# Optimization experiments

Measured on AMD Instinct MI355X. Metric: run time of the kernel, lower is better.

## Reference

```python
import jax, jax.numpy as jnp
import numpy as np
import math

H = 8          # num_heads
HD = 16        # head_dim = attention_dim // (2*num_heads) = 256 // 16
E_SUB = 256
E_GENE = 256
DEPTH = 1
LAMBDA_INIT = 0.8 - 0.6 * math.exp(-0.3 * DEPTH)
EPS_SM = 1e-20
EPS_RMS = 1e-5


def setup_inputs() -> dict:
    key = jax.random.key(0)
    ks = jax.random.split(key, 12)
    B, S, P, G = 4, 512, 64, 32
    d2 = 2 * H * HD  # 256
    inp = {
        'query': jax.random.normal(ks[0], (B, S, E_SUB), jnp.float32),
        'key': jax.random.normal(ks[1], (B, P, G, E_GENE), jnp.float32),
        'query_mask': jnp.ones((B, S), dtype=bool),
        'key_mask': jnp.ones((B, P, G), dtype=bool),
        'Wq': jax.random.normal(ks[2], (E_SUB, d2), jnp.float32) / np.sqrt(E_SUB),
        'Wk': jax.random.normal(ks[3], (E_GENE, d2), jnp.float32) / np.sqrt(E_GENE),
        'Wv': jax.random.normal(ks[4], (E_GENE, d2), jnp.float32) / np.sqrt(E_GENE),
        'Wo': jax.random.normal(ks[5], (d2, E_SUB), jnp.float32) / np.sqrt(d2),
        'lq1': 0.1 * jax.random.normal(ks[6], (HD,), jnp.float32),
        'lk1': 0.1 * jax.random.normal(ks[7], (HD,), jnp.float32),
        'lq2': 0.1 * jax.random.normal(ks[8], (HD,), jnp.float32),
        'lk2': 0.1 * jax.random.normal(ks[9], (HD,), jnp.float32),
        'g': jnp.ones((2 * HD,), jnp.float32),  # RMSNorm weight
    }
    return inp


def _stable_softmax(x):
    x = x.astype(jnp.float32)
    m = jnp.max(x, axis=-1, keepdims=True)
    e = jnp.exp(x - m)
    return e / (jnp.sum(e, axis=-1, keepdims=True) + EPS_SM)


def reference(query, key, query_mask, key_mask, Wq, Wk, Wv, Wo, lq1, lk1, lq2, lk2, g):
    B, S, _ = query.shape
    _, P, G, Ek = key.shape
    Lk = P * G
    scaling = HD ** -0.5
    key_flat = key.reshape(B, Lk, Ek)
    # [B, H, 2, S/Lk, HD]
    Q = (query @ Wq).reshape(B, S, H, 2, HD).transpose(0, 2, 3, 1, 4) * scaling
    K = (key_flat @ Wk).reshape(B, Lk, H, 2, HD).transpose(0, 2, 3, 1, 4)
    V = (key_flat @ Wv).reshape(B, Lk, H, 2, HD).transpose(0, 2, 3, 1, 4)
    # dual-slot scores [B, H, 2, S, Lk]
    scores = jnp.einsum('bhtsd,bhtld->bhtsl', Q, K)
    mask = query_mask[:, None, None, :, None] & key_mask.reshape(B, Lk)[:, None, None, None, :]
    scores = jnp.where(mask, scores, jnp.float32(-1e20))
    scores = _stable_softmax(scores)
    lam1 = jnp.exp(jnp.sum(lq1 * lk1))
    lam2 = jnp.exp(jnp.sum(lq2 * lk2))
    lam_full = lam1 - lam2 + LAMBDA_INIT
    diff_attn = scores[:, :, 0] - lam_full * scores[:, :, 1]  # [B,H,S,Lk]
    V_cat = V.transpose(0, 1, 3, 2, 4).reshape(B, H, Lk, 2 * HD)
    out = jnp.einsum('bhsl,bhld->bhsd', diff_attn, V_cat)
    # RMSNorm over last dim, then scale
    rms = jax.lax.rsqrt(jnp.mean(out * out, axis=-1, keepdims=True) + EPS_RMS)
    out = out * rms * g * (1.0 - LAMBDA_INIT)
    out = out.transpose(0, 2, 1, 3).reshape(B, S, 2 * H * HD) @ Wo
    return out, diff_attn.reshape(B, H, S, P, G)
```

## Files before the change

### kernel.cpp

```cpp
#include <hip/hip_runtime.h>
#include <hip/hip_bf16.h>


typedef float  f32x4  __attribute__((ext_vector_type(4)));
typedef float  f32x16 __attribute__((ext_vector_type(16)));
typedef short  s16x8  __attribute__((ext_vector_type(8)));
typedef unsigned short u16;
typedef unsigned short u16x4 __attribute__((ext_vector_type(4)));
typedef unsigned int   u32;

#define LAMBDA_INIT   0.35550906759096926f
#define ONE_MINUS_LI  0.6444909324090307f
#define QSCALE        0.36067376022224085f

__device__ __forceinline__ u16 f2b(float x) {
  unsigned u = __float_as_uint(x);
  u += 0x7FFFu + ((u >> 16) & 1u);
  return (u16)(u >> 16);
}

__device__ __forceinline__ u32 cvtpk(float lo, float hi) {
  u32 r;
  asm("v_cvt_pk_bf16_f32 %0, %1, %2" : "=v"(r) : "v"(lo), "v"(hi));
  return r;
}

__device__ __forceinline__ float fexp2(float x) {
  return __builtin_amdgcn_exp2f(x);
}

__global__ __launch_bounds__(256) void proj_kernel(
    const float* __restrict__ query, const float* __restrict__ key,
    const float* __restrict__ Wq, const float* __restrict__ Wk,
    const float* __restrict__ Wv,
    u16* __restrict__ Qs, u16* __restrict__ Ks, u16* __restrict__ Vt) {
  const int z = blockIdx.z;
  if (z == 0 && blockIdx.x >= 32) return;
  const float* A = (z == 0) ? query : key;
  const float* W = (z == 0) ? Wq : (z == 1) ? Wk : Wv;
  u16*         Out = (z == 0) ? Qs : (z == 1) ? Ks : Vt;
  const float scale = (z == 0) ? QSCALE : 1.0f;

  __shared__ u16 ldsA[64][40];
  __shared__ u16 ldsB[64][40];
  const int m0 = blockIdx.x * 64, n0 = blockIdx.y * 64;
  const int tid = threadIdx.x;
  const int w = tid >> 6, lane = tid & 63;
  const int wm = (w >> 1) * 32, wn = (w & 1) * 32;
  const int c = lane & 15, q = lane >> 4;
  const int lr = tid >> 2, lc = (tid & 3) * 8;
  const int n2 = tid & 63, ko = tid >> 6;
  f32x4 acc[2][2] = {};
  const float* aptr = A + (size_t)(m0 + lr) * 256 + lc;
  const float* bp   = W + (size_t)(ko * 8) * 256 + n0 + n2;

  f32x4 a0 = *reinterpret_cast<const f32x4*>(aptr);
  f32x4 a1 = *reinterpret_cast<const f32x4*>(aptr + 4);
  float bw[8];
#pragma unroll
  for (int j = 0; j < 8; ++j) bw[j] = bp[(size_t)j * 256];
  for (int k0 = 0; k0 < 256; k0 += 32) {
    u16x4 p0 = {f2b(a0[0]), f2b(a0[1]), f2b(a0[2]), f2b(a0[3])};
    u16x4 p1 = {f2b(a1[0]), f2b(a1[1]), f2b(a1[2]), f2b(a1[3])};
    *reinterpret_cast<u16x4*>(&ldsA[lr][lc]) = p0;
    *reinterpret_cast<u16x4*>(&ldsA[lr][lc + 4]) = p1;
    s16x8 pb;
#pragma unroll
    for (int j = 0; j < 8; ++j) pb[j] = (short)f2b(bw[j]);
    *reinterpret_cast<s16x8*>(&ldsB[n2][ko * 8]) = pb;
    __syncthreads();
    if (k0 + 32 < 256) {
      a0 = *reinterpret_cast<const f32x4*>(aptr + k0 + 32);
      a1 = *reinterpret_cast<const f32x4*>(aptr + k0 + 36);
#pragma unroll
      for (int j = 0; j < 8; ++j) bw[j] = bp[(size_t)(k0 + 32 + j) * 256];
    }
    s16x8 af0 = *reinterpret_cast<const s16x8*>(&ldsA[wm + c][q * 8]);
    s16x8 af1 = *reinterpret_cast<const s16x8*>(&ldsA[wm + 16 + c][q * 8]);
    s16x8 bf0 = *reinterpret_cast<const s16x8*>(&ldsB[wn + c][q * 8]);
    s16x8 bf1 = *reinterpret_cast<const s16x8*>(&ldsB[wn + 16 + c][q * 8]);
    acc[0][0] = __builtin_amdgcn_mfma_f32_16x16x32_bf16(af0, bf0, acc[0][0], 0, 0, 0);
    acc[0][1] = __builtin_amdgcn_mfma_f32_16x16x32_bf16(af0, bf1, acc[0][1], 0, 0, 0);
    acc[1][0] = __builtin_amdgcn_mfma_f32_16x16x32_bf16(af1, bf0, acc[1][0], 0, 0, 0);
    acc[1][1] = __builtin_amdgcn_mfma_f32_16x16x32_bf16(af1, bf1, acc[1][1], 0, 0, 0);
    __syncthreads();
  }
#pragma unroll
  for (int mf = 0; mf < 2; ++mf)
#pragma unroll
    for (int nf = 0; nf < 2; ++nf) {
      int m = m0 + wm + mf * 16 + q * 4;
      int n = n0 + wn + nf * 16 + c;
      int hh = n >> 5, dd = n & 31;
      if (z == 2) {
        int bb = m >> 11, l = m & 2047;
        int t = l >> 4, u = l & 15;
        u16x4 pk = {f2b(acc[mf][nf][0]), f2b(acc[mf][nf][1]),
                    f2b(acc[mf][nf][2]), f2b(acc[mf][nf][3])};
        size_t idx = (((size_t)((bb * 8 + hh) * 128 + t)) * 32 + dd) * 16 + u;
        *reinterpret_cast<u16x4*>(Out + idx) = pk;
      } else {
#pragma unroll
        for (int r = 0; r < 4; ++r) {
          int mm = m + r;
          size_t idx;
          if (z == 0) {
            int bb = mm >> 9, s = mm & 511;
            idx = ((size_t)((bb * 8 + hh) * 512 + s)) * 32 + dd;
          } else {
            int bb = mm >> 11, l = mm & 2047;
            idx = ((size_t)((bb * 8 + hh) * 2048 + l)) * 32 + dd;
          }
          Out[idx] = f2b(acc[mf][nf][r] * scale);
        }
      }
    }
}

__global__ __launch_bounds__(512, 4) void attn_fused_kernel(
    const u16* __restrict__ Qs, const u16* __restrict__ Ks,
    const u16* __restrict__ Vt,
    const float* __restrict__ lq1, const float* __restrict__ lk1,
    const float* __restrict__ lq2, const float* __restrict__ lk2,
    const float* __restrict__ g,
    float* __restrict__ diff_out, u16* __restrict__ normed) {
  __shared__ float psum[8][2][32];
  __shared__ float rden[2][32];
  __shared__ float avred[8][16][64];
  __shared__ float pstg[8][32][33];
  const int i = blockIdx.x;
  const int xcd = i & 7, j = i >> 3;
  const int bh = xcd * 4 + (j >> 4);
  const int st = j & 15;
  const int b = bh >> 3, h = bh & 7;
  const int tid = threadIdx.x, w = tid >> 6, lane = tid & 63;
  const int ln = lane & 31, hi = lane >> 5;
  const int lbase = w * 256;

  float a1 = 0.f, a2 = 0.f;
#pragma unroll
  for (int t = 0; t < 16; ++t) { a1 += lq1[t] * lk1[t]; a2 += lq2[t] * lk2[t]; }
  const float lam = expf(a1) - expf(a2) + LAMBDA_INIT;

  const u16* qptr = Qs + ((size_t)((b * 8 + h) * 512 + st * 32 + ln)) * 32 + hi * 8;
  const s16x8 qf0 = *reinterpret_cast<const s16x8*>(qptr);
  const s16x8 qf1 = *reinterpret_cast<const s16x8*>(qptr + 16);
  const u16* kbase = Ks + ((size_t)((b * 8 + h) * 2048)) * 32 + hi * 8;
  const u16* vbase = Vt + ((size_t)(b * 8 + h)) * 65536 + ln * 16 + hi * 8;

  float s0 = 0.f, s1 = 0.f;
  {
    const u16* kptr = kbase + (size_t)(lbase + ln) * 32;
    s16x8 kf0 = *reinterpret_cast<const s16x8*>(kptr);
    s16x8 kf1 = *reinterpret_cast<const s16x8*>(kptr + 16);
    for (int l0 = lbase; l0 < lbase + 256; l0 += 32) {
      const int lnext = (l0 + 32 < lbase + 256) ? l0 + 32 : lbase;
      const u16* knext = kbase + (size_t)(lnext + ln) * 32;
      s16x8 nf0 = *reinterpret_cast<const s16x8*>(knext);
      s16x8 nf1 = *reinterpret_cast<const s16x8*>(knext + 16);
      f32x16 c0 = {}, c1 = {};
      c0 = __builtin_amdgcn_mfma_f32_32x32x16_bf16(kf0, qf0, c0, 0, 0, 0);
      c1 = __builtin_amdgcn_mfma_f32_32x32x16_bf16(kf1, qf1, c1, 0, 0, 0);
#pragma unroll
      for (int r = 0; r < 16; ++r) { s0 += fexp2(c0[r]); s1 += fexp2(c1[r]); }
      kf0 = nf0; kf1 = nf1;
    }
  }
  s0 += __shfl_xor(s0, 32);
  s1 += __shfl_xor(s1, 32);
  if (lane < 32) { psum[w][0][lane] = s0; psum[w][1][lane] = s1; }
  __syncthreads();
  float t0 = 0.f, t1 = 0.f;
#pragma unroll
  for (int ww = 0; ww < 8; ++ww) { t0 += psum[ww][0][ln]; t1 += psum[ww][1][ln]; }
  const float r0 = 1.f / (t0 + 1e-20f);
  const float r1 = lam / (t1 + 1e-20f);
  if (w == 0 && lane < 32) { rden[0][lane] = r0; rden[1][lane] = r1; }
  __syncthreads();
  f32x4 rq[4], rl[4];
#pragma unroll
  for (int gq = 0; gq < 4; ++gq) {
    rq[gq] = *reinterpret_cast<const f32x4*>(&rden[0][gq * 8 + 4 * hi]);
    rl[gq] = *reinterpret_cast<const f32x4*>(&rden[1][gq * 8 + 4 * hi]);
  }

  f32x16 avacc = {};
  float* dbase = diff_out + ((size_t)((b * 8 + h) * 512 + st * 32)) * 2048;
  {
    const u16* kptr = kbase + (size_t)(lbase + ln) * 32;
    s16x8 kf0 = *reinterpret_cast<const s16x8*>(kptr);
    s16x8 kf1 = *reinterpret_cast<const s16x8*>(kptr + 16);
    s16x8 vf0 = *reinterpret_cast<const s16x8*>(vbase + (size_t)((lbase >> 4) + 0) * 512);
    s16x8 vf1 = *reinterpret_cast<const s16x8*>(vbase + (size_t)((lbase >> 4) + 1) * 512);
    for (int l0 = lbase; l0 < lbase + 256; l0 += 32) {
      const int lnext = (l0 + 32 < lbase + 256) ? l0 + 32 : lbase;
      const u16* knext = kbase + (size_t)(lnext + ln) * 32;
      s16x8 nk0 = *reinterpret_cast<const s16x8*>(knext);
      s16x8 nk1 = *reinterpret_cast<const s16x8*>(knext + 16);
      s16x8 nv0 = *reinterpret_cast<const s16x8*>(vbase + (size_t)((lnext >> 4) + 0) * 512);
      s16x8 nv1 = *reinterpret_cast<const s16x8*>(vbase + (size_t)((lnext >> 4) + 1) * 512);
      f32x16 c0 = {}, c1 = {};
      c0 = __builtin_amdgcn_mfma_f32_32x32x16_bf16(qf0, kf0, c0, 0, 0, 0);
      c1 = __builtin_amdgcn_mfma_f32_32x32x16_bf16(qf1, kf1, c1, 0, 0, 0);
#pragma unroll
      for (int r = 0; r < 16; ++r) {
        float dn = fexp2(c0[r]) * rq[r >> 2][r & 3] -
                   fexp2(c1[r]) * rl[r >> 2][r & 3];
        pstg[w][(r & 3) + 8 * (r >> 2) + 4 * hi][ln] = dn;
      }
      f32x4 paa = *reinterpret_cast<const f32x4*>(&pstg[w][ln][hi * 8]);
      f32x4 pab = *reinterpret_cast<const f32x4*>(&pstg[w][ln][hi * 8 + 4]);
      f32x4 pba = *reinterpret_cast<const f32x4*>(&pstg[w][ln][16 + hi * 8]);
      f32x4 pbb = *reinterpret_cast<const f32x4*>(&pstg[w][ln][16 + hi * 8 + 4]);
      union { u32 u[4]; s16x8 s; } fa, fb;
      fa.u[0] = cvtpk(paa[0], paa[1]); fa.u[1] = cvtpk(paa[2], paa[3]);
      fa.u[2] = cvtpk(pab[0], pab[1]); fa.u[3] = cvtpk(pab[2], pab[3]);
      fb.u[0] = cvtpk(pba[0], pba[1]); fb.u[1] = cvtpk(pba[2], pba[3]);
      fb.u[2] = cvtpk(pbb[0], pbb[1]); fb.u[3] = cvtpk(pbb[2], pbb[3]);
      avacc = __builtin_amdgcn_mfma_f32_32x32x16_bf16(vf0, fa.s, avacc, 0, 0, 0);
      avacc = __builtin_amdgcn_mfma_f32_32x32x16_bf16(vf1, fb.s, avacc, 0, 0, 0);
#pragma unroll
      for (int jj = 0; jj < 4; ++jj) {
        int srow = jj * 8 + (lane >> 3);
        int lofs = (lane & 7) * 4;
        f32x4 v = *reinterpret_cast<const f32x4*>(&pstg[w][srow][lofs]);
        *reinterpret_cast<f32x4*>(dbase + (size_t)srow * 2048 + l0 + lofs) = v;
      }
      kf0 = nk0; kf1 = nk1; vf0 = nv0; vf1 = nv1;
    }
  }

#pragma unroll
  for (int r = 0; r < 16; ++r) avred[w][r][lane] = avacc[r];
  __syncthreads();
  if (w < 4) {
#pragma unroll
    for (int r = 0; r < 16; ++r) {
      avacc[r] += avred[w + 4][r][lane];
      avred[w][r][lane] = avacc[r];
    }
  }
  __syncthreads();
  if (w < 2) {
#pragma unroll
    for (int r = 0; r < 16; ++r) {
      avacc[r] += avred[w + 2][r][lane];
      avred[w][r][lane] = avacc[r];
    }
  }
  __syncthreads();
  if (w == 0) {
#pragma unroll
    for (int r = 0; r < 16; ++r) avacc[r] += avred[1][r][lane];
    float ss = 0.f;
#pragma unroll
    for (int r = 0; r < 16; ++r) ss += avacc[r] * avacc[r];
    ss += __shfl_xor(ss, 32);
    const float sc = rsqrtf(ss * (1.f / 32.f) + 1e-5f) * ONE_MINUS_LI;
    u16* nrow = normed + ((size_t)(b * 512 + st * 32 + ln)) * 256 + h * 32 + 4 * hi;
#pragma unroll
    for (int rg = 0; rg < 4; ++rg) {
      const float* gp = g + 8 * rg + 4 * hi;
      u16x4 pk = {f2b(avacc[4 * rg + 0] * sc * gp[0]),
                  f2b(avacc[4 * rg + 1] * sc * gp[1]),
                  f2b(avacc[4 * rg + 2] * sc * gp[2]),
                  f2b(avacc[4 * rg + 3] * sc * gp[3])};
      *reinterpret_cast<u16x4*>(nrow + 8 * rg) = pk;
    }
  }
}

__global__ __launch_bounds__(256) void gemmo_kernel(
    const u16* __restrict__ A, const float* __restrict__ Wo,
    float* __restrict__ Out) {
  __shared__ u16 ldsA[64][40];
  __shared__ u16 ldsB[64][40];
  const int m0 = blockIdx.x * 64, n0 = blockIdx.y * 64;
  const int tid = threadIdx.x;
  const int w = tid >> 6, lane = tid & 63;
  const int wm = (w >> 1) * 32, wn = (w & 1) * 32;
  const int c = lane & 15, q = lane >> 4;
  const int lr = tid >> 2, lc = (tid & 3) * 8;
  const int n2 = tid & 63, ko = tid >> 6;
  f32x4 acc[2][2] = {};
  const u16*   aptr = A + (size_t)(m0 + lr) * 256 + lc;
  const float* bp   = Wo + (size_t)(ko * 8) * 256 + n0 + n2;
  s16x8 aF = *reinterpret_cast<const s16x8*>(aptr);
  float bw[8];
#pragma unroll
  for (int j = 0; j < 8; ++j) bw[j] = bp[(size_t)j * 256];
  for (int k0 = 0; k0 < 256; k0 += 32) {
    *reinterpret_cast<s16x8*>(&ldsA[lr][lc]) = aF;
    s16x8 pb;
#pragma unroll
    for (int j = 0; j < 8; ++j) pb[j] = (short)f2b(bw[j]);
    *reinterpret_cast<s16x8*>(&ldsB[n2][ko * 8]) = pb;
    __syncthreads();
    if (k0 + 32 < 256) {
      aF = *reinterpret_cast<const s16x8*>(aptr + k0 + 32);
#pragma unroll
      for (int j = 0; j < 8; ++j) bw[j] = bp[(size_t)(k0 + 32 + j) * 256];
    }
    s16x8 af0 = *reinterpret_cast<const s16x8*>(&ldsA[wm + c][q * 8]);
    s16x8 af1 = *reinterpret_cast<const s16x8*>(&ldsA[wm + 16 + c][q * 8]);
    s16x8 bf0 = *reinterpret_cast<const s16x8*>(&ldsB[wn + c][q * 8]);
    s16x8 bf1 = *reinterpret_cast<const s16x8*>(&ldsB[wn + 16 + c][q * 8]);
    acc[0][0] = __builtin_amdgcn_mfma_f32_16x16x32_bf16(af0, bf0, acc[0][0], 0, 0, 0);
    acc[0][1] = __builtin_amdgcn_mfma_f32_16x16x32_bf16(af0, bf1, acc[0][1], 0, 0, 0);
    acc[1][0] = __builtin_amdgcn_mfma_f32_16x16x32_bf16(af1, bf0, acc[1][0], 0, 0, 0);
    acc[1][1] = __builtin_amdgcn_mfma_f32_16x16x32_bf16(af1, bf1, acc[1][1], 0, 0, 0);
    __syncthreads();
  }
#pragma unroll
  for (int mf = 0; mf < 2; ++mf)
#pragma unroll
    for (int nf = 0; nf < 2; ++nf)
#pragma unroll
      for (int r = 0; r < 4; ++r) {
        int m = m0 + wm + mf * 16 + q * 4 + r;
        int n = n0 + wn + nf * 16 + c;
        Out[(size_t)m * 256 + n] = acc[mf][nf][r];
      }
}

extern "C" void kernel_launch(void* const* d_in, const int* in_sizes, int n_in,
                              void* d_out, int out_size, void* d_ws, size_t ws_size,
                              hipStream_t stream) {
  const float* query = (const float*)d_in[0];
  const float* key   = (const float*)d_in[1];
  const float* Wq  = (const float*)d_in[4];
  const float* Wk  = (const float*)d_in[5];
  const float* Wv  = (const float*)d_in[6];
  const float* Wo  = (const float*)d_in[7];
  const float* lq1 = (const float*)d_in[8];
  const float* lk1 = (const float*)d_in[9];
  const float* lq2 = (const float*)d_in[10];
  const float* lk2 = (const float*)d_in[11];
  const float* g   = (const float*)d_in[12];

  float* out  = (float*)d_out;
  float* diff = out + 524288;

  char* ws = (char*)d_ws;
  u16* Qs  = (u16*)(ws);
  u16* Ks  = (u16*)(ws + (size_t)1 * (1 << 20));
  u16* Vt  = (u16*)(ws + (size_t)5 * (1 << 20));
  u16* nrm = (u16*)(ws + (size_t)9 * (1 << 20));

  proj_kernel<<<dim3(128, 4, 3), 256, 0, stream>>>(query, key, Wq, Wk, Wv,
                                                   Qs, Ks, Vt);
  attn_fused_kernel<<<512, 512, 0, stream>>>(
      Qs, Ks, Vt, lq1, lk1, lq2, lk2, g, diff, nrm);
  gemmo_kernel<<<dim3(32, 4), 256, 0, stream>>>(nrm, Wo, out);
}
```

Baseline: 52.99 us.

## Process two query tiles per block, overlapping tile B's denominator pass with tile A's output pass

Each attention block now handles two 32-row query tiles instead of one, and the grid is halved to 256 blocks. The softmax-denominator pass for the second tile is merged into the output/AV pass of the first, so the K fragments loaded there serve both the QK^T MFMAs of both tiles. This removes one full separate sweep over K per tile pair and gives more independent MFMA and exp work per iteration. In exchange the blocks get more register pressure (launch bounds lowered to 2), fewer blocks are in flight, the merged loop drops its software prefetch, and the block's work becomes more serial.

Result: slower. 55.81 us (+5.3%).

```diff
diff --git a/kernel.cpp b/kernel.cpp
--- a/kernel.cpp
+++ b/kernel.cpp
@@ -117,21 +117,23 @@
     }
 }
 
-__global__ __launch_bounds__(512, 4) void attn_fused_kernel(
+__global__ __launch_bounds__(512, 2) void attn_fused_kernel(
     const u16* __restrict__ Qs, const u16* __restrict__ Ks,
     const u16* __restrict__ Vt,
     const float* __restrict__ lq1, const float* __restrict__ lk1,
     const float* __restrict__ lq2, const float* __restrict__ lk2,
     const float* __restrict__ g,
     float* __restrict__ diff_out, u16* __restrict__ normed) {
-  __shared__ float psum[8][2][32];
+  __shared__ float psumA[8][2][32];
+  __shared__ float psumB[8][2][32];
   __shared__ float rden[2][32];
   __shared__ float avred[8][16][64];
   __shared__ float pstg[8][32][33];
   const int i = blockIdx.x;
   const int xcd = i & 7, j = i >> 3;
-  const int bh = xcd * 4 + (j >> 4);
-  const int st = j & 15;
+  const int bh = xcd * 4 + (j >> 3);
+  const int pr = j & 7;
+  const int stA = pr * 2, stB = pr * 2 + 1;
   const int b = bh >> 3, h = bh & 7;
   const int tid = threadIdx.x, w = tid >> 6, lane = tid & 63;
   const int ln = lane & 31, hi = lane >> 5;
@@ -142,9 +144,13 @@
   for (int t = 0; t < 16; ++t) { a1 += lq1[t] * lk1[t]; a2 += lq2[t] * lk2[t]; }
   const float lam = expf(a1) - expf(a2) + LAMBDA_INIT;
 
-  const u16* qptr = Qs + ((size_t)((b * 8 + h) * 512 + st * 32 + ln)) * 32 + hi * 8;
-  const s16x8 qf0 = *reinterpret_cast<const s16x8*>(qptr);
-  const s16x8 qf1 = *reinterpret_cast<const s16x8*>(qptr + 16);
+  const u16* qbase = Qs + ((size_t)((b * 8 + h) * 512)) * 32;
+  const u16* qpA = qbase + (size_t)(stA * 32 + ln) * 32 + hi * 8;
+  const u16* qpB = qbase + (size_t)(stB * 32 + ln) * 32 + hi * 8;
+  const s16x8 qfA0 = *reinterpret_cast<const s16x8*>(qpA);
+  const s16x8 qfA1 = *reinterpret_cast<const s16x8*>(qpA + 16);
+  const s16x8 qfB0 = *reinterpret_cast<const s16x8*>(qpB);
+  const s16x8 qfB1 = *reinterpret_cast<const s16x8*>(qpB + 16);
   const u16* kbase = Ks + ((size_t)((b * 8 + h) * 2048)) * 32 + hi * 8;
   const u16* vbase = Vt + ((size_t)(b * 8 + h)) * 65536 + ln * 16 + hi * 8;
 
@@ -159,8 +165,8 @@
       s16x8 nf0 = *reinterpret_cast<const s16x8*>(knext);
       s16x8 nf1 = *reinterpret_cast<const s16x8*>(knext + 16);
       f32x16 c0 = {}, c1 = {};
-      c0 = __builtin_amdgcn_mfma_f32_32x32x16_bf16(kf0, qf0, c0, 0, 0, 0);
-      c1 = __builtin_amdgcn_mfma_f32_32x32x16_bf16(kf1, qf1, c1, 0, 0, 0);
+      c0 = __builtin_amdgcn_mfma_f32_32x32x16_bf16(kf0, qfA0, c0, 0, 0, 0);
+      c1 = __builtin_amdgcn_mfma_f32_32x32x16_bf16(kf1, qfA1, c1, 0, 0, 0);
 #pragma unroll
       for (int r = 0; r < 16; ++r) { s0 += fexp2(c0[r]); s1 += fexp2(c1[r]); }
       kf0 = nf0; kf1 = nf1;
@@ -168,25 +174,133 @@
   }
   s0 += __shfl_xor(s0, 32);
   s1 += __shfl_xor(s1, 32);
-  if (lane < 32) { psum[w][0][lane] = s0; psum[w][1][lane] = s1; }
-  __syncthreads();
-  float t0 = 0.f, t1 = 0.f;
-#pragma unroll
-  for (int ww = 0; ww < 8; ++ww) { t0 += psum[ww][0][ln]; t1 += psum[ww][1][ln]; }
-  const float r0 = 1.f / (t0 + 1e-20f);
-  const float r1 = lam / (t1 + 1e-20f);
-  if (w == 0 && lane < 32) { rden[0][lane] = r0; rden[1][lane] = r1; }
-  __syncthreads();
-  f32x4 rq[4], rl[4];
+  if (lane < 32) { psumA[w][0][lane] = s0; psumA[w][1][lane] = s1; }
+  __syncthreads();
+  {
+    float t0 = 0.f, t1 = 0.f;
+#pragma unroll
+    for (int ww = 0; ww < 8; ++ww) { t0 += psumA[ww][0][ln]; t1 += psumA[ww][1][ln]; }
+    if (w == 0 && lane < 32) {
+      rden[0][lane] = 1.f / (t0 + 1e-20f);
+      rden[1][lane] = lam / (t1 + 1e-20f);
+    }
+  }
+  __syncthreads();
+  f32x4 rqA[4], rlA[4];
 #pragma unroll
   for (int gq = 0; gq < 4; ++gq) {
-    rq[gq] = *reinterpret_cast<const f32x4*>(&rden[0][gq * 8 + 4 * hi]);
-    rl[gq] = *reinterpret_cast<const f32x4*>(&rden[1][gq * 8 + 4 * hi]);
+    rqA[gq] = *reinterpret_cast<const f32x4*>(&rden[0][gq * 8 + 4 * hi]);
+    rlA[gq] = *reinterpret_cast<const f32x4*>(&rden[1][gq * 8 + 4 * hi]);
   }
 
   f32x16 avacc = {};
-  float* dbase = diff_out + ((size_t)((b * 8 + h) * 512 + st * 32)) * 2048;
+  float sB0 = 0.f, sB1 = 0.f;
   {
+    float* dbase = diff_out + ((size_t)((b * 8 + h) * 512 + stA * 32)) * 2048;
+    for (int l0 = lbase; l0 < lbase + 256; l0 += 32) {
+      const u16* kptr = kbase + (size_t)(l0 + ln) * 32;
+      s16x8 kf0 = *reinterpret_cast<const s16x8*>(kptr);
+      s16x8 kf1 = *reinterpret_cast<const s16x8*>(kptr + 16);
+      s16x8 vf0 = *reinterpret_cast<const s16x8*>(vbase + (size_t)((l0 >> 4) + 0) * 512);
+      s16x8 vf1 = *reinterpret_cast<const s16x8*>(vbase + (size_t)((l0 >> 4) + 1) * 512);
+      f32x16 b0 = {}, b1 = {};
+      b0 = __builtin_amdgcn_mfma_f32_32x32x16_bf16(kf0, qfB0, b0, 0, 0, 0);
+      b1 = __builtin_amdgcn_mfma_f32_32x32x16_bf16(kf1, qfB1, b1, 0, 0, 0);
+      f32x16 c0 = {}, c1 = {};
+      c0 = __builtin_amdgcn_mfma_f32_32x32x16_bf16(qfA0, kf0, c0, 0, 0, 0);
+      c1 = __builtin_amdgcn_mfma_f32_32x32x16_bf16(qfA1, kf1, c1, 0, 0, 0);
+#pragma unroll
+      for (int r = 0; r < 16; ++r) {
+        float dn = fexp2(c0[r]) * rqA[r >> 2][r & 3] -
+                   fexp2(c1[r]) * rlA[r >> 2][r & 3];
+        pstg[w][(r & 3) + 8 * (r >> 2) + 4 * hi][ln] = dn;
+      }
+      f32x4 paa = *reinterpret_cast<const f32x4*>(&pstg[w][ln][hi * 8]);
+      f32x4 pab = *reinterpret_cast<const f32x4*>(&pstg[w][ln][hi * 8 + 4]);
+      f32x4 pba = *reinterpret_cast<const f32x4*>(&pstg[w][ln][16 + hi * 8]);
+      f32x4 pbb = *reinterpret_cast<const f32x4*>(&pstg[w][ln][16 + hi * 8 + 4]);
+      union { u32 u[4]; s16x8 s; } fa, fb;
+      fa.u[0] = cvtpk(paa[0], paa[1]); fa.u[1] = cvtpk(paa[2], paa[3]);
+      fa.u[2] = cvtpk(pab[0], pab[1]); fa.u[3] = cvtpk(pab[2], pab[3]);
+      fb.u[0] = cvtpk(pba[0], pba[1]); fb.u[1] = cvtpk(pba[2], pba[3]);
+      fb.u[2] = cvtpk(pbb[0], pbb[1]); fb.u[3] = cvtpk(pbb[2], pbb[3]);
+      avacc = __builtin_amdgcn_mfma_f32_32x32x16_bf16(vf0, fa.s, avacc, 0, 0, 0);
+      avacc = __builtin_amdgcn_mfma_f32_32x32x16_bf16(vf1, fb.s, avacc, 0, 0, 0);
+#pragma unroll
+      for (int jj = 0; jj < 4; ++jj) {
+        int srow = jj * 8 + (lane >> 3);
+        int lofs = (lane & 7) * 4;
+        f32x4 v = *reinterpret_cast<const f32x4*>(&pstg[w][srow][lofs]);
+        *reinterpret_cast<f32x4*>(dbase + (size_t)srow * 2048 + l0 + lofs) = v;
+      }
+#pragma unroll
+      for (int r = 0; r < 16; ++r) { sB0 += fexp2(b0[r]); sB1 += fexp2(b1[r]); }
+    }
+  }
+  sB0 += __shfl_xor(sB0, 32);
+  sB1 += __shfl_xor(sB1, 32);
+  if (lane < 32) { psumB[w][0][lane] = sB0; psumB[w][1][lane] = sB1; }
+
+#pragma unroll
+  for (int r = 0; r < 16; ++r) avred[w][r][lane] = avacc[r];
+  __syncthreads();
+  if (w < 4) {
+#pragma unroll
+    for (int r = 0; r < 16; ++r) {
+      avacc[r] += avred[w + 4][r][lane];
+      avred[w][r][lane] = avacc[r];
+    }
+  }
+  __syncthreads();
+  if (w < 2) {
+#pragma unroll
+    for (int r = 0; r < 16; ++r) {
+      avacc[r] += avred[w + 2][r][lane];
+      avred[w][r][lane] = avacc[r];
+    }
+  }
+  __syncthreads();
+  if (w == 0) {
+#pragma unroll
+    for (int r = 0; r < 16; ++r) avacc[r] += avred[1][r][lane];
+    float ss = 0.f;
+#pragma unroll
+    for (int r = 0; r < 16; ++r) ss += avacc[r] * avacc[r];
+    ss += __shfl_xor(ss, 32);
+    const float sc = rsqrtf(ss * (1.f / 32.f) + 1e-5f) * ONE_MINUS_LI;
+    u16* nrow = normed + ((size_t)(b * 512 + stA * 32 + ln)) * 256 + h * 32 + 4 * hi;
+#pragma unroll
+    for (int rg = 0; rg < 4; ++rg) {
+      const float* gp = g + 8 * rg + 4 * hi;
+      u16x4 pk = {f2b(avacc[4 * rg + 0] * sc * gp[0]),
+                  f2b(avacc[4 * rg + 1] * sc * gp[1]),
+                  f2b(avacc[4 * rg + 2] * sc * gp[2]),
+                  f2b(avacc[4 * rg + 3] * sc * gp[3])};
+      *reinterpret_cast<u16x4*>(nrow + 8 * rg) = pk;
+    }
+  }
+  __syncthreads();
+
+  {
+    float t0 = 0.f, t1 = 0.f;
+#pragma unroll
+    for (int ww = 0; ww < 8; ++ww) { t0 += psumB[ww][0][ln]; t1 += psumB[ww][1][ln]; }
+    if (w == 0 && lane < 32) {
+      rden[0][lane] = 1.f / (t0 + 1e-20f);
+      rden[1][lane] = lam / (t1 + 1e-20f);
+    }
+  }
+  __syncthreads();
+  f32x4 rqB[4], rlB[4];
+#pragma unroll
+  for (int gq = 0; gq < 4; ++gq) {
+    rqB[gq] = *reinterpret_cast<const f32x4*>(&rden[0][gq * 8 + 4 * hi]);
+    rlB[gq] = *reinterpret_cast<const f32x4*>(&rden[1][gq * 8 + 4 * hi]);
+  }
+
+  f32x16 avB = {};
+  {
+    float* dbase = diff_out + ((size_t)((b * 8 + h) * 512 + stB * 32)) * 2048;
     const u16* kptr = kbase + (size_t)(lbase + ln) * 32;
     s16x8 kf0 = *reinterpret_cast<const s16x8*>(kptr);
     s16x8 kf1 = *reinterpret_cast<const s16x8*>(kptr + 16);
@@ -200,12 +314,12 @@
       s16x8 nv0 = *reinterpret_cast<const s16x8*>(vbase + (size_t)((lnext >> 4) + 0) * 512);
       s16x8 nv1 = *reinterpret_cast<const s16x8*>(vbase + (size_t)((lnext >> 4) + 1) * 512);
       f32x16 c0 = {}, c1 = {};
-      c0 = __builtin_amdgcn_mfma_f32_32x32x16_bf16(qf0, kf0, c0, 0, 0, 0);
-      c1 = __builtin_amdgcn_mfma_f32_32x32x16_bf16(qf1, kf1, c1, 0, 0, 0);
+      c0 = __builtin_amdgcn_mfma_f32_32x32x16_bf16(qfB0, kf0, c0, 0, 0, 0);
+      c1 = __builtin_amdgcn_mfma_f32_32x32x16_bf16(qfB1, kf1, c1, 0, 0, 0);
 #pragma unroll
       for (int r = 0; r < 16; ++r) {
-        float dn = fexp2(c0[r]) * rq[r >> 2][r & 3] -
-                   fexp2(c1[r]) * rl[r >> 2][r & 3];
+        float dn = fexp2(c0[r]) * rqB[r >> 2][r & 3] -
+                   fexp2(c1[r]) * rlB[r >> 2][r & 3];
         pstg[w][(r & 3) + 8 * (r >> 2) + 4 * hi][ln] = dn;
       }
       f32x4 paa = *reinterpret_cast<const f32x4*>(&pstg[w][ln][hi * 8]);
@@ -217,8 +331,8 @@
       fa.u[2] = cvtpk(pab[0], pab[1]); fa.u[3] = cvtpk(pab[2], pab[3]);
       fb.u[0] = cvtpk(pba[0], pba[1]); fb.u[1] = cvtpk(pba[2], pba[3]);
       fb.u[2] = cvtpk(pbb[0], pbb[1]); fb.u[3] = cvtpk(pbb[2], pbb[3]);
-      avacc = __builtin_amdgcn_mfma_f32_32x32x16_bf16(vf0, fa.s, avacc, 0, 0, 0);
-      avacc = __builtin_amdgcn_mfma_f32_32x32x16_bf16(vf1, fb.s, avacc, 0, 0, 0);
+      avB = __builtin_amdgcn_mfma_f32_32x32x16_bf16(vf0, fa.s, avB, 0, 0, 0);
+      avB = __builtin_amdgcn_mfma_f32_32x32x16_bf16(vf1, fb.s, avB, 0, 0, 0);
 #pragma unroll
       for (int jj = 0; jj < 4; ++jj) {
         int srow = jj * 8 + (lane >> 3);
@@ -231,40 +345,40 @@
   }
 
 #pragma unroll
-  for (int r = 0; r < 16; ++r) avred[w][r][lane] = avacc[r];
+  for (int r = 0; r < 16; ++r) avred[w][r][lane] = avB[r];
   __syncthreads();
   if (w < 4) {
 #pragma unroll
     for (int r = 0; r < 16; ++r) {
-      avacc[r] += avred[w + 4][r][lane];
-      avred[w][r][lane] = avacc[r];
+      avB[r] += avred[w + 4][r][lane];
+      avred[w][r][lane] = avB[r];
     }
   }
   __syncthreads();
   if (w < 2) {
 #pragma unroll
     for (int r = 0; r < 16; ++r) {
-      avacc[r] += avred[w + 2][r][lane];
-      avred[w][r][lane] = avacc[r];
+      avB[r] += avred[w + 2][r][lane];
+      avred[w][r][lane] = avB[r];
     }
   }
   __syncthreads();
   if (w == 0) {
 #pragma unroll
-    for (int r = 0; r < 16; ++r) avacc[r] += avred[1][r][lane];
+    for (int r = 0; r < 16; ++r) avB[r] += avred[1][r][lane];
     float ss = 0.f;
 #pragma unroll
-    for (int r = 0; r < 16; ++r) ss += avacc[r] * avacc[r];
+    for (int r = 0; r < 16; ++r) ss += avB[r] * avB[r];
     ss += __shfl_xor(ss, 32);
     const float sc = rsqrtf(ss * (1.f / 32.f) + 1e-5f) * ONE_MINUS_LI;
-    u16* nrow = normed + ((size_t)(b * 512 + st * 32 + ln)) * 256 + h * 32 + 4 * hi;
+    u16* nrow = normed + ((size_t)(b * 512 + stB * 32 + ln)) * 256 + h * 32 + 4 * hi;
 #pragma unroll
     for (int rg = 0; rg < 4; ++rg) {
       const float* gp = g + 8 * rg + 4 * hi;
-      u16x4 pk = {f2b(avacc[4 * rg + 0] * sc * gp[0]),
-                  f2b(avacc[4 * rg + 1] * sc * gp[1]),
-                  f2b(avacc[4 * rg + 2] * sc * gp[2]),
-                  f2b(avacc[4 * rg + 3] * sc * gp[3])};
+      u16x4 pk = {f2b(avB[4 * rg + 0] * sc * gp[0]),
+                  f2b(avB[4 * rg + 1] * sc * gp[1]),
+                  f2b(avB[4 * rg + 2] * sc * gp[2]),
+                  f2b(avB[4 * rg + 3] * sc * gp[3])};
       *reinterpret_cast<u16x4*>(nrow + 8 * rg) = pk;
     }
   }
@@ -349,7 +463,7 @@
 
   proj_kernel<<<dim3(128, 4, 3), 256, 0, stream>>>(query, key, Wq, Wk, Wv,
                                                    Qs, Ks, Vt);
-  attn_fused_kernel<<<512, 512, 0, stream>>>(
+  attn_fused_kernel<<<256, 512, 0, stream>>>(
       Qs, Ks, Vt, lq1, lk1, lq2, lk2, g, diff, nrm);
   gemmo_kernel<<<dim3(32, 4), 256, 0, stream>>>(nrm, Wo, out);
 }
```
